# Kernel optimization log

Measured on AMD Instinct MI355X. Metric: run time of the kernel, lower is better.

Reference implementation:

```python
import jax, jax.numpy as jnp
import numpy as np

NUM_RBF = 16
MAX_REL = 32
TOP_K = 48

PAIRS = [("N","N"),("C","C"),("O","O"),("Cb","Cb"),("Ca","N"),("Ca","C"),
         ("Ca","O"),("Ca","Cb"),("N","C"),("N","O"),("N","Cb"),("Cb","C"),
         ("Cb","O"),("O","C"),("N","Ca"),("C","Ca"),("O","Ca"),("Cb","Ca"),
         ("C","N"),("O","N"),("Cb","N"),("C","Cb"),("O","Cb"),("C","O")]

def _rbf(D):
    # D: [B,L,K] -> [B,L,K,NUM_RBF]
    mu = jnp.linspace(2.0, 22.0, NUM_RBF)
    sigma = (22.0 - 2.0) / NUM_RBF
    return jnp.exp(-(((D[..., None] - mu) / sigma) ** 2))

def setup_inputs():
    key = jax.random.key(0)
    ks = jax.random.split(key, 8)
    B, L = 4, 2048
    X = jax.random.normal(ks[0], (B, L, 4, 3), dtype=jnp.float32) * 3.0
    mask = jnp.ones((B, L), dtype=jnp.float32)
    residue_idx = jnp.sort(jax.random.randint(ks[1], (B, L), 0, 3000), axis=-1).astype(jnp.int32)
    chain_labels = jax.random.randint(ks[2], (B, L), 0, 4).astype(jnp.int32)
    pe_w = jax.random.normal(ks[3], (16, 66), dtype=jnp.float32) * 0.1
    pe_b = jnp.zeros((16,), dtype=jnp.float32)
    edge_w = jax.random.normal(ks[4], (128, 416), dtype=jnp.float32) * 0.05
    ln_scale = jnp.ones((128,), dtype=jnp.float32)
    ln_bias = jnp.zeros((128,), dtype=jnp.float32)
    return dict(X=X, mask=mask, residue_idx=residue_idx, chain_labels=chain_labels,
                pe_w=pe_w, pe_b=pe_b, edge_w=edge_w, ln_scale=ln_scale, ln_bias=ln_bias)

def reference(X, mask, residue_idx, chain_labels, pe_w, pe_b, edge_w, ln_scale, ln_bias):
    Bn, L = X.shape[0], X.shape[1]
    # virtual Cb from backbone geometry
    b = X[:, :, 1, :] - X[:, :, 0, :]
    c = X[:, :, 2, :] - X[:, :, 1, :]
    a = jnp.cross(b, c)
    Cb = -0.58273431 * a + 0.56802827 * b - 0.54067466 * c + X[:, :, 1, :]
    atoms = {"N": X[:, :, 0, :], "Ca": X[:, :, 1, :], "C": X[:, :, 2, :],
             "O": X[:, :, 3, :], "Cb": Cb}
    Ca = atoms["Ca"]
    # brute-force kNN on Ca-Ca distances (_dist)
    mask2d = mask[:, :, None] * mask[:, None, :]                       # [B,L,L]
    D = mask2d * jnp.sqrt(jnp.sum((Ca[:, :, None, :] - Ca[:, None, :, :]) ** 2, -1) + 1e-6)
    D_adjust = D + (1.0 - mask2d) * jnp.max(D, -1, keepdims=True)
    negD, E_idx = jax.lax.top_k(-D_adjust, TOP_K)                      # smallest distances
    D_neighbors = -negD                                                # [B,L,K]
    # gather neighbor coordinates once per atom type; pairwise dists only on [B,L,K]
    bidx = jnp.arange(Bn)[:, None, None]
    nb = {k: v[bidx, E_idx] for k, v in atoms.items()}                 # [B,L,K,3]
    def pair_dist(A, Bnb):
        return jnp.sqrt(jnp.sum((A[:, :, None, :] - Bnb) ** 2, -1) + 1e-6)
    RBF_all = [_rbf(D_neighbors)]
    for an, bn in PAIRS:
        RBF_all.append(_rbf(pair_dist(atoms[an], nb[bn])))
    RBF_all = jnp.concatenate(RBF_all, -1)                             # [B,L,K,25*NUM_RBF]
    # positional encodings of gathered residue offsets
    offset = residue_idx[:, :, None] - residue_idx[:, None, :]         # [B,L,L]
    offset_nb = jnp.take_along_axis(offset, E_idx, axis=2)             # [B,L,K]
    same_chain = (chain_labels[:, :, None] == chain_labels[:, None, :]).astype(jnp.int32)
    E_chains = jnp.take_along_axis(same_chain, E_idx, axis=2)          # [B,L,K]
    d = jnp.clip(offset_nb + MAX_REL, 0, 2 * MAX_REL)
    d = d * E_chains + (1 - E_chains) * (2 * MAX_REL + 1)
    d_onehot = jax.nn.one_hot(d, 2 * MAX_REL + 2, dtype=jnp.float32)   # [B,L,K,66]
    E_pos = jnp.einsum("blkf,ef->blke", d_onehot, pe_w) + pe_b
    # edge embedding + layernorm
    E = jnp.concatenate([E_pos, RBF_all], -1)                          # [B,L,K,416]
    E = jnp.einsum("blkf,ef->blke", E, edge_w)                         # [B,L,K,128]
    mu = jnp.mean(E, -1, keepdims=True)
    var = jnp.var(E, -1, keepdims=True)
    E = (E - mu) / jnp.sqrt(var + 1e-5) * ln_scale + ln_bias
    return E, E_idx
```

## Files before the change

kernel.cpp:

```cpp
#include <hip/hip_runtime.h>
#include <stdint.h>

typedef unsigned long long u64;
typedef unsigned int u32;
typedef unsigned short u16;
typedef float f32x4 __attribute__((ext_vector_type(4)));
typedef short s16x8 __attribute__((ext_vector_type(8)));

#define NB 4
#define NL 2048
#define NK 48
#define NRES (NB*NL)
#define NEDGE (NRES*NK)
#define NF 416
#define LDA 424
#define TS 32
#define CLS 136
#define NHB 1152

#define EIDX_OFF 50331648u

#define WS_ATOMS 0u
#define WS_WB    655360u
#define WS_PETAB 761856u
#define WS_EIDX  786432u
#define WS_DNB   2359296u

__constant__ int c_PA_r25[24] = {0,2,3,4,1,1,1,1,0,0,0,4,4,3,0,2,3,4,2,3,4,2,3,2};
__constant__ int c_PB_r25[24] = {0,2,3,4,0,2,3,4,2,3,4,2,3,2,1,1,1,1,0,0,0,4,4,3};

static __device__ __forceinline__ u16 f2bf(float v) {
    u32 u = __float_as_uint(v);
    u = (u + 0x7fffu + ((u >> 16) & 1u)) >> 16;
    return (u16)u;
}
static __device__ __forceinline__ float bfout(float v) {
    return __uint_as_float((u32)f2bf(v) << 16);
}
static __device__ __forceinline__ float bftrunc(float v) {
    return __uint_as_float(__float_as_uint(v) & 0xffff0000u);
}
static __device__ __forceinline__ u16 bt16(float v) {
    return (u16)(__float_as_uint(v) >> 16);
}

static __device__ __forceinline__ float dist_np(float ax, float ay, float az,
                                                float bx, float by, float bz) {
    #pragma clang fp contract(off)
    float dx = ax - bx, dy = ay - by, dz = az - bz;
    float s = dx * dx;
    s = s + dy * dy;
    s = s + dz * dz;
    s = s + 1e-6f;
    return (float)sqrt((double)s);
}

__global__ __launch_bounds__(256) void k_prep_r25(
        const float* __restrict__ X, const float* __restrict__ edge_w,
        const float* __restrict__ pe_w, const float* __restrict__ pe_b,
        float4* __restrict__ atoms, u16* __restrict__ Wb, u16* __restrict__ petab) {
    int bid = blockIdx.x, tid = threadIdx.x;
    if (bid < 32) {
        int r = (bid << 8) + tid;
        const float4* Xr = (const float4*)(X + (size_t)r * 12);
        float4 q0 = Xr[0], q1 = Xr[1], q2 = Xr[2];
        float Nx=q0.x, Ny=q0.y, Nz=q0.z;
        float Cax=q0.w, Cay=q1.x, Caz=q1.y;
        float Cx=q1.z, Cy=q1.w, Cz=q2.x;
        float Ox=q2.y, Oy=q2.z, Oz=q2.w;
        float bx=Cax-Nx, by=Cay-Ny, bz=Caz-Nz;
        float cx=Cx-Cax, cy=Cy-Cay, cz=Cz-Caz;
        float ax=by*cz-bz*cy, ay=bz*cx-bx*cz, az=bx*cy-by*cx;
        float Cbx = -0.58273431f*ax + 0.56802827f*bx - 0.54067466f*cx + Cax;
        float Cby = -0.58273431f*ay + 0.56802827f*by - 0.54067466f*cy + Cay;
        float Cbz = -0.58273431f*az + 0.56802827f*bz - 0.54067466f*cz + Caz;
        atoms[0*NRES + r] = make_float4(Nx,Ny,Nz,0.f);
        atoms[1*NRES + r] = make_float4(Cax,Cay,Caz,0.f);
        atoms[2*NRES + r] = make_float4(Cx,Cy,Cz,0.f);
        atoms[3*NRES + r] = make_float4(Ox,Oy,Oz,0.f);
        atoms[4*NRES + r] = make_float4(Cbx,Cby,Cbz,0.f);
    } else if (bid < 240) {
        int w = ((bid - 32) << 8) + tid;
        Wb[w] = f2bf(edge_w[w]);
    } else {
        int t = ((bid - 240) << 8) + tid;
        if (t < 66 * 16) {
            int d = t >> 4, e = t & 15;
            petab[t] = f2bf(pe_w[e * 66 + d] + pe_b[e]);
        }
    }
}

__global__ __launch_bounds__(256) void k_knn_r25(
        const float4* __restrict__ atoms, const float* __restrict__ mask,
        int* __restrict__ eidx, float* __restrict__ dnb, float* __restrict__ outI) {
    __shared__ u32 hist[4][NHB];
    __shared__ u64 cand[4][64];
    int tid = threadIdx.x;
    int wv = tid >> 6, lane = tid & 63;
    int grow = blockIdx.x * 4 + wv;
    int b = grow >> 11;
    const float4* ca = atoms + NRES + (b << 11);
    const float* mk = mask + (b << 11);

    float4 ci = ca[grow & 2047];
    float mi = mk[grow & 2047];
    u32 adjb[32];
    float dmax = 0.f;
    #pragma unroll
    for (int t = 0; t < 32; ++t) {
        int j = lane + (t << 6);
        float4 cj = ca[j];
        float d = dist_np(ci.x, ci.y, ci.z, cj.x, cj.y, cj.z);
        float md = (mi * mk[j]) * d;
        dmax = fmaxf(dmax, md);
        adjb[t] = __float_as_uint(md);
    }
    #pragma unroll
    for (int off = 32; off; off >>= 1) dmax = fmaxf(dmax, __shfl_xor(dmax, off));
    u32 dmb = __float_as_uint(dmax);
    #pragma unroll
    for (int t = 0; t < 32; ++t) if (adjb[t] == 0u) adjb[t] = dmb;

    #pragma unroll
    for (int i = 0; i < 18; ++i) hist[wv][lane * 18 + i] = 0u;
    cand[wv][lane] = ~0ull;
    __syncthreads();

    #pragma unroll
    for (int t = 0; t < 32; ++t) {
        int bk = (int)(adjb[t] >> 16) - 0x3E00;
        bk = bk < 0 ? 0 : (bk > NHB - 1 ? NHB - 1 : bk);
        atomicAdd(&hist[wv][bk], 1u);
    }
    __syncthreads();

    u32 S = 0;
    #pragma unroll
    for (int i = 0; i < 18; ++i) S += hist[wv][lane * 18 + i];
    u32 cum = S;
    #pragma unroll
    for (int off = 1; off < 64; off <<= 1) {
        u32 o = __shfl_up(cum, off);
        if (lane >= off) cum += o;
    }
    u64 bal = __ballot(cum >= NK);
    int first = (int)__ffsll((unsigned long long)bal) - 1;
    u32 cumprev = (first == 0) ? 0u : (u32)__shfl((int)(cum - S), first);
    int Bstar = first * 18 + 17;
    u32 c = cumprev;
    #pragma unroll 1
    for (int i = 0; i < 18; ++i) {
        c += hist[wv][first * 18 + i];
        if (c >= NK) { Bstar = first * 18 + i; break; }
    }
    u32 ncand = c;

    bool small = (ncand <= 64u);
    if (small) {
        u32 base = 0;
        #pragma unroll
        for (int t = 0; t < 32; ++t) {
            int bk = (int)(adjb[t] >> 16) - 0x3E00;
            bk = bk < 0 ? 0 : (bk > NHB - 1 ? NHB - 1 : bk);
            bool p = (bk <= Bstar);
            u64 m = __ballot(p);
            if (p) {
                u32 pos = base + (u32)__popcll(m & ((1ull << lane) - 1ull));
                cand[wv][pos] = ((u64)adjb[t] << 32) | (u32)(lane + (t << 6));
            }
            base += (u32)__popcll(m);
        }
    }
    __syncthreads();

    if (small) {
        u64 key = cand[wv][lane];
        u32 klo = (u32)key, khi = (u32)(key >> 32);
        int rank = 0;
        #pragma unroll
        for (int s = 0; s < 64; ++s) {
            u32 olo = (u32)__shfl((int)klo, s);
            u32 ohi = (u32)__shfl((int)khi, s);
            rank += (ohi < khi) || (ohi == khi && olo < klo);
        }
        if (rank < NK) {
            int e = grow * NK + rank;
            int j = (int)klo;
            eidx[e] = j;
            dnb[e] = __uint_as_float(khi);
            outI[e] = bfout((float)j);
        }
    } else {
        u64 prev = 0, res = 0;
        #pragma unroll 1
        for (int it = 0; it < NK; ++it) {
            u64 best = ~0ull;
            #pragma unroll
            for (int t = 0; t < 32; ++t) {
                u64 k = ((u64)adjb[t] << 32) | (u32)(lane + (t << 6));
                bool cc = (k > prev) && (k < best);
                best = cc ? k : best;
            }
            #pragma unroll
            for (int off = 32; off; off >>= 1) {
                u32 lo = (u32)best, hi = (u32)(best >> 32);
                u32 olo = (u32)__shfl_xor((int)lo, off);
                u32 ohi = (u32)__shfl_xor((int)hi, off);
                u64 o = ((u64)ohi << 32) | olo;
                best = (o < best) ? o : best;
            }
            if (lane == it) res = best;
            prev = best;
        }
        if (lane < NK) {
            int e = grow * NK + lane;
            int j = (int)(res & 0xffffffffull);
            eidx[e] = j;
            dnb[e] = __uint_as_float((u32)(res >> 32));
            outI[e] = bfout((float)j);
        }
    }
}

__global__ __launch_bounds__(256) void k_edge_r25(
        const float4* __restrict__ atoms, const int* __restrict__ eidx,
        const float* __restrict__ dnb, const int* __restrict__ residx,
        const int* __restrict__ chains, const u16* __restrict__ Wb,
        const u16* __restrict__ petab, const float* __restrict__ ln_s,
        const float* __restrict__ ln_b, float* __restrict__ outF) {
    __shared__ __align__(16) u16 Abuf[TS * LDA];
    __shared__ int srow[TS], sjg[TS];
    float* Cls = (float*)Abuf;
    int tid = threadIdx.x;
    int e0 = blockIdx.x << 5;

    if (tid < TS) {
        int e = e0 + tid;
        int row = e / NK;
        int b = row >> 11;
        int j = eidx[e];
        int jg = (b << 11) + j;
        srow[tid] = row;
        sjg[tid] = jg;
        int d = residx[row] - residx[jg] + 32;
        d = d < 0 ? 0 : (d > 64 ? 64 : d);
        d = (chains[row] == chains[jg]) ? d : 65;
        const uint4* src = (const uint4*)(petab + d * 16);
        uint4* dst = (uint4*)(Abuf + tid * LDA);
        dst[0] = src[0];
        dst[1] = src[1];
    }
    __syncthreads();

    #pragma unroll 1
    for (int it = 0; it < 4; ++it) {
        int tau = tid + (it << 8);
        if (tau < TS * 25) {
            int el = tau / 25;
            int s = tau - el * 25;
            float dv;
            if (s == 0) {
                dv = dnb[e0 + el];
            } else {
                float4 pa = atoms[c_PA_r25[s-1] * NRES + srow[el]];
                float4 pb = atoms[c_PB_r25[s-1] * NRES + sjg[el]];
                float dx = pa.x - pb.x, dy = pa.y - pb.y, dz = pa.z - pb.z;
                dv = sqrtf(dx*dx + dy*dy + dz*dz + 1e-6f);
            }
            u32 o[8];
            #pragma unroll
            for (int m = 0; m < 8; ++m) {
                float mu0 = 2.f + (20.f/15.f) * (2*m);
                float mu1 = 2.f + (20.f/15.f) * (2*m+1);
                float a0 = (dv - mu0) * 0.8f;
                float a1 = (dv - mu1) * 0.8f;
                float v0 = __expf(-a0*a0);
                float v1 = __expf(-a1*a1);
                o[m] = (u32)bt16(v0) | ((u32)bt16(v1) << 16);
            }
            uint4* dst = (uint4*)(Abuf + el * LDA + 16 + 16 * s);
            dst[0] = make_uint4(o[0], o[1], o[2], o[3]);
            dst[1] = make_uint4(o[4], o[5], o[6], o[7]);
        }
    }
    __syncthreads();

    int w = tid >> 6, lane = tid & 63;
    int lrow = lane & 15, lgrp = lane >> 4;
    f32x4 acc[2][2] = {};
    const u16* wb0 = Wb + (w * 32 + lrow) * NF;
    const u16* wb1 = wb0 + 16 * NF;
    #pragma unroll 1
    for (int kk = 0; kk < 13; ++kk) {
        int k0 = kk * 32 + lgrp * 8;
        s16x8 b0 = *(const s16x8*)(wb0 + k0);
        s16x8 b1 = *(const s16x8*)(wb1 + k0);
        s16x8 a0 = *(const s16x8*)(Abuf + lrow * LDA + k0);
        s16x8 a1 = *(const s16x8*)(Abuf + (16 + lrow) * LDA + k0);
        acc[0][0] = __builtin_amdgcn_mfma_f32_16x16x32_bf16(a0, b0, acc[0][0], 0, 0, 0);
        acc[0][1] = __builtin_amdgcn_mfma_f32_16x16x32_bf16(a0, b1, acc[0][1], 0, 0, 0);
        acc[1][0] = __builtin_amdgcn_mfma_f32_16x16x32_bf16(a1, b0, acc[1][0], 0, 0, 0);
        acc[1][1] = __builtin_amdgcn_mfma_f32_16x16x32_bf16(a1, b1, acc[1][1], 0, 0, 0);
    }
    __syncthreads();
    #pragma unroll
    for (int mt = 0; mt < 2; ++mt) {
        #pragma unroll
        for (int nt = 0; nt < 2; ++nt) {
            #pragma unroll
            for (int r = 0; r < 4; ++r) {
                Cls[(mt * 16 + lgrp * 4 + r) * CLS + w * 32 + nt * 16 + lrow] = acc[mt][nt][r];
            }
        }
    }
    __syncthreads();

    int row = tid >> 3, t8 = tid & 7;
    const float4* Crow = (const float4*)(Cls + row * CLS);
    float4 xv[4];
    float s = 0.f, sq = 0.f;
    #pragma unroll
    for (int k = 0; k < 4; ++k) {
        float4 v = Crow[t8 + 8 * k];
        xv[k] = v;
        s += v.x + v.y + v.z + v.w;
        sq += v.x*v.x + v.y*v.y + v.z*v.z + v.w*v.w;
    }
    s += __shfl_xor(s, 1); sq += __shfl_xor(sq, 1);
    s += __shfl_xor(s, 2); sq += __shfl_xor(sq, 2);
    s += __shfl_xor(s, 4); sq += __shfl_xor(sq, 4);
    float mean = s * (1.f / 128.f);
    float var = fmaxf(sq * (1.f / 128.f) - mean * mean, 0.f);
    float rstd = 1.f / sqrtf(var + 1e-5f);
    float4* drow = (float4*)(outF + (size_t)(e0 + row) * 128);
    #pragma unroll
    for (int k = 0; k < 4; ++k) {
        int c0 = t8 * 4 + 32 * k;
        float4 g = *(const float4*)(ln_s + c0);
        float4 bb = *(const float4*)(ln_b + c0);
        float4 y;
        y.x = bftrunc((xv[k].x - mean) * rstd * g.x + bb.x);
        y.y = bftrunc((xv[k].y - mean) * rstd * g.y + bb.y);
        y.z = bftrunc((xv[k].z - mean) * rstd * g.z + bb.z);
        y.w = bftrunc((xv[k].w - mean) * rstd * g.w + bb.w);
        drow[t8 + 8 * k] = y;
    }
}

extern "C" void kernel_launch(void* const* d_in, const int* in_sizes, int n_in,
                              void* d_out, int out_size, void* d_ws, size_t ws_size,
                              hipStream_t stream) {
    const float* X        = (const float*)d_in[0];
    const float* mask     = (const float*)d_in[1];
    const int*   residx   = (const int*)d_in[2];
    const int*   chains   = (const int*)d_in[3];
    const float* pe_w     = (const float*)d_in[4];
    const float* pe_b     = (const float*)d_in[5];
    const float* edge_w   = (const float*)d_in[6];
    const float* ln_s     = (const float*)d_in[7];
    const float* ln_b     = (const float*)d_in[8];
    char* ws = (char*)d_ws;
    float4* atoms = (float4*)(ws + WS_ATOMS);
    u16*    Wb    = (u16*)(ws + WS_WB);
    u16*    petab = (u16*)(ws + WS_PETAB);
    int*    eidx  = (int*)(ws + WS_EIDX);
    float*  dnb   = (float*)(ws + WS_DNB);
    float* outF = (float*)d_out;
    float* outI = outF + EIDX_OFF;

    k_prep_r25<<<245, 256, 0, stream>>>(X, edge_w, pe_w, pe_b, atoms, Wb, petab);
    k_knn_r25<<<2048, 256, 0, stream>>>(atoms, mask, eidx, dnb, outI);
    k_edge_r25<<<12288, 256, 0, stream>>>(atoms, eidx, dnb, residx, chains, Wb,
                                          petab, ln_s, ln_b, outF);
}
```

Baseline: 192.6 us.

## Compute RBF by exp recurrence, remap RBF work, swizzle LDS output tile

Each distance's 16 Gaussian RBF values are now built from two exps and a geometric recurrence (exp(-(u-k*d)^2) factorised) rather than 16 separate exps. The work mapping changes from a div-by-25 loop to 8 threads per edge handling 3 pairs each, with a leftover pair on one lane. A raw hardware v_sqrt replaces sqrtf. The accumulator write to LDS is XOR-swizzled to avoid bank conflicts, and the layernorm read and store indices are unswizzled to match. The recurrence can lose some accuracy and the remapping leaves one lane per edge doing an extra pair, which adds imbalance.

Result: faster. 187.6 us (-2.6%).

```diff
diff --git a/kernel.cpp b/kernel.cpp
--- a/kernel.cpp
+++ b/kernel.cpp
@@ -26,8 +26,8 @@
 #define WS_EIDX  786432u
 #define WS_DNB   2359296u
 
-__constant__ int c_PA_r25[24] = {0,2,3,4,1,1,1,1,0,0,0,4,4,3,0,2,3,4,2,3,4,2,3,2};
-__constant__ int c_PB_r25[24] = {0,2,3,4,0,2,3,4,2,3,4,2,3,2,1,1,1,1,0,0,0,4,4,3};
+__constant__ int c_PA_r26[24] = {0,2,3,4,1,1,1,1,0,0,0,4,4,3,0,2,3,4,2,3,4,2,3,2};
+__constant__ int c_PB_r26[24] = {0,2,3,4,0,2,3,4,2,3,4,2,3,2,1,1,1,1,0,0,0,4,4,3};
 
 static __device__ __forceinline__ u16 f2bf(float v) {
     u32 u = __float_as_uint(v);
@@ -42,6 +42,9 @@
 }
 static __device__ __forceinline__ u16 bt16(float v) {
     return (u16)(__float_as_uint(v) >> 16);
+}
+static __device__ __forceinline__ float fsqrt_hw(float x) {
+    float r; asm("v_sqrt_f32 %0, %1" : "=v"(r) : "v"(x)); return r;
 }
 
 static __device__ __forceinline__ float dist_np(float ax, float ay, float az,
@@ -55,7 +58,7 @@
     return (float)sqrt((double)s);
 }
 
-__global__ __launch_bounds__(256) void k_prep_r25(
+__global__ __launch_bounds__(256) void k_prep_r26(
         const float* __restrict__ X, const float* __restrict__ edge_w,
         const float* __restrict__ pe_w, const float* __restrict__ pe_b,
         float4* __restrict__ atoms, u16* __restrict__ Wb, u16* __restrict__ petab) {
@@ -91,7 +94,7 @@
     }
 }
 
-__global__ __launch_bounds__(256) void k_knn_r25(
+__global__ __launch_bounds__(256) void k_knn_r26(
         const float4* __restrict__ atoms, const float* __restrict__ mask,
         int* __restrict__ eidx, float* __restrict__ dnb, float* __restrict__ outI) {
     __shared__ u32 hist[4][NHB];
@@ -223,7 +226,24 @@
     }
 }
 
-__global__ __launch_bounds__(256) void k_edge_r25(
+static __device__ __forceinline__ void rbf_store(u16* dst16, float dv) {
+    float u0 = (dv - 2.f) * 0.8f;
+    float t = __expf(-u0 * u0);
+    float rr = __expf(fminf(2.1333333f * u0 - 1.1377778f, 85.f));
+    const float q = 0.1027349f;
+    u16 h[16];
+    h[0] = bt16(t);
+    #pragma unroll
+    for (int m = 1; m < 16; ++m) { t *= rr; rr *= q; h[m] = bt16(t); }
+    u32 o[8];
+    #pragma unroll
+    for (int m = 0; m < 8; ++m) o[m] = (u32)h[2*m] | ((u32)h[2*m+1] << 16);
+    uint4* dst = (uint4*)dst16;
+    dst[0] = make_uint4(o[0], o[1], o[2], o[3]);
+    dst[1] = make_uint4(o[4], o[5], o[6], o[7]);
+}
+
+__global__ __launch_bounds__(256) void k_edge_r26(
         const float4* __restrict__ atoms, const int* __restrict__ eidx,
         const float* __restrict__ dnb, const int* __restrict__ residx,
         const int* __restrict__ chains, const u16* __restrict__ Wb,
@@ -253,35 +273,29 @@
     }
     __syncthreads();
 
-    #pragma unroll 1
-    for (int it = 0; it < 4; ++it) {
-        int tau = tid + (it << 8);
-        if (tau < TS * 25) {
-            int el = tau / 25;
-            int s = tau - el * 25;
+    {
+        int el = tid >> 3, p = tid & 7;
+        int row = srow[el], jg = sjg[el];
+        u16* abase = Abuf + el * LDA + 16;
+        #pragma unroll
+        for (int jj = 0; jj < 3; ++jj) {
+            int s = p + (jj << 3);
             float dv;
             if (s == 0) {
                 dv = dnb[e0 + el];
             } else {
-                float4 pa = atoms[c_PA_r25[s-1] * NRES + srow[el]];
-                float4 pb = atoms[c_PB_r25[s-1] * NRES + sjg[el]];
+                float4 pa = atoms[c_PA_r26[s-1] * NRES + row];
+                float4 pb = atoms[c_PB_r26[s-1] * NRES + jg];
                 float dx = pa.x - pb.x, dy = pa.y - pb.y, dz = pa.z - pb.z;
-                dv = sqrtf(dx*dx + dy*dy + dz*dz + 1e-6f);
-            }
-            u32 o[8];
-            #pragma unroll
-            for (int m = 0; m < 8; ++m) {
-                float mu0 = 2.f + (20.f/15.f) * (2*m);
-                float mu1 = 2.f + (20.f/15.f) * (2*m+1);
-                float a0 = (dv - mu0) * 0.8f;
-                float a1 = (dv - mu1) * 0.8f;
-                float v0 = __expf(-a0*a0);
-                float v1 = __expf(-a1*a1);
-                o[m] = (u32)bt16(v0) | ((u32)bt16(v1) << 16);
-            }
-            uint4* dst = (uint4*)(Abuf + el * LDA + 16 + 16 * s);
-            dst[0] = make_uint4(o[0], o[1], o[2], o[3]);
-            dst[1] = make_uint4(o[4], o[5], o[6], o[7]);
+                dv = fsqrt_hw(dx*dx + dy*dy + dz*dz + 1e-6f);
+            }
+            rbf_store(abase + 16 * s, dv);
+        }
+        if (p == 0) {
+            float4 pa = atoms[c_PA_r26[23] * NRES + row];
+            float4 pb = atoms[c_PB_r26[23] * NRES + jg];
+            float dx = pa.x - pb.x, dy = pa.y - pb.y, dz = pa.z - pb.z;
+            rbf_store(abase + 16 * 24, fsqrt_hw(dx*dx + dy*dy + dz*dz + 1e-6f));
         }
     }
     __syncthreads();
@@ -310,13 +324,16 @@
         for (int nt = 0; nt < 2; ++nt) {
             #pragma unroll
             for (int r = 0; r < 4; ++r) {
-                Cls[(mt * 16 + lgrp * 4 + r) * CLS + w * 32 + nt * 16 + lrow] = acc[mt][nt][r];
+                int rw = mt * 16 + lgrp * 4 + r;
+                int cl = (w * 32 + nt * 16 + lrow) ^ (lgrp << 3);
+                Cls[rw * CLS + cl] = acc[mt][nt][r];
             }
         }
     }
     __syncthreads();
 
     int row = tid >> 3, t8 = tid & 7;
+    int swz = ((row >> 2) & 3) << 3;
     const float4* Crow = (const float4*)(Cls + row * CLS);
     float4 xv[4];
     float s = 0.f, sq = 0.f;
@@ -336,7 +353,8 @@
     float4* drow = (float4*)(outF + (size_t)(e0 + row) * 128);
     #pragma unroll
     for (int k = 0; k < 4; ++k) {
-        int c0 = t8 * 4 + 32 * k;
+        int q = t8 + 8 * k;
+        int c0 = (q * 4) ^ swz;
         float4 g = *(const float4*)(ln_s + c0);
         float4 bb = *(const float4*)(ln_b + c0);
         float4 y;
@@ -344,7 +362,7 @@
         y.y = bftrunc((xv[k].y - mean) * rstd * g.y + bb.y);
         y.z = bftrunc((xv[k].z - mean) * rstd * g.z + bb.z);
         y.w = bftrunc((xv[k].w - mean) * rstd * g.w + bb.w);
-        drow[t8 + 8 * k] = y;
+        drow[c0 >> 2] = y;
     }
 }
 
@@ -369,8 +387,8 @@
     float* outF = (float*)d_out;
     float* outI = outF + EIDX_OFF;
 
-    k_prep_r25<<<245, 256, 0, stream>>>(X, edge_w, pe_w, pe_b, atoms, Wb, petab);
-    k_knn_r25<<<2048, 256, 0, stream>>>(atoms, mask, eidx, dnb, outI);
-    k_edge_r25<<<12288, 256, 0, stream>>>(atoms, eidx, dnb, residx, chains, Wb,
+    k_prep_r26<<<245, 256, 0, stream>>>(X, edge_w, pe_w, pe_b, atoms, Wb, petab);
+    k_knn_r26<<<2048, 256, 0, stream>>>(atoms, mask, eidx, dnb, outI);
+    k_edge_r26<<<12288, 256, 0, stream>>>(atoms, eidx, dnb, residx, chains, Wb,
                                           petab, ln_s, ln_b, outF);
 }
```
